# Kernel optimization log

Hardware: AMD Instinct MI355X
Metric: run time of the kernel (lower is better)

The kernel has to match this reference:

```python
import jax, jax.numpy as jnp
import numpy as np

HIDDEN = 1024
HEADS = 16
HEAD_DIM = HIDDEN // HEADS
SCALE = HEAD_DIM ** -0.5


def setup_inputs() -> dict:
    key = jax.random.key(0)
    ks = jax.random.split(key, 7)
    B, N, T = 4, 64, 128
    x = jax.random.normal(ks[0], (B * N, T, HIDDEN), dtype=jnp.float32)
    bvecs = jax.random.normal(ks[1], (B, T, 3), dtype=jnp.float32)
    w_std = HIDDEN ** -0.5
    qkv_w = jax.random.normal(ks[2], (HIDDEN, 3 * HIDDEN), dtype=jnp.float32) * w_std
    qkv_b = jnp.zeros((3 * HIDDEN,), dtype=jnp.float32)
    proj_w = jax.random.normal(ks[3], (HIDDEN, HIDDEN), dtype=jnp.float32) * w_std
    proj_b = jnp.zeros((HIDDEN,), dtype=jnp.float32)
    angular_bias_scale = jnp.ones((1,), dtype=jnp.float32)
    return {"x": x, "bvecs": bvecs, "qkv_w": qkv_w, "qkv_b": qkv_b,
            "proj_w": proj_w, "proj_b": proj_b,
            "angular_bias_scale": angular_bias_scale}


def reference(x, bvecs, qkv_w, qkv_b, proj_w, proj_b, angular_bias_scale):
    BN, T, D = x.shape
    B = bvecs.shape[0]
    N = BN // B
    # QKV projection -> (3, BN, H, T, hd)
    qkv = (x @ qkv_w + qkv_b).reshape(BN, T, 3, HEADS, HEAD_DIM)
    qkv = jnp.transpose(qkv, (2, 0, 3, 1, 4))
    q, k, v = qkv[0], qkv[1], qkv[2]
    # normalize b-vectors and compute per-batch angular cosine similarity (B, T, T)
    bvecs_n = bvecs / (jnp.linalg.norm(bvecs, axis=-1, keepdims=True) + 1e-6)
    cos_sim = jnp.clip(jnp.einsum('bid,bjd->bij', bvecs_n, bvecs_n), -1.0, 1.0)
    # repeat across the N patches per batch -> (BN, 1, T, T)
    angular_bias = jnp.repeat(cos_sim, N, axis=0)[:, None, :, :]
    attn_logits = jnp.einsum('bhid,bhjd->bhij', q, k) * SCALE
    attn = jax.nn.softmax(attn_logits + angular_bias_scale * angular_bias, axis=-1)
    out = jnp.einsum('bhij,bhjd->bhid', attn, v)
    out = jnp.transpose(out, (0, 2, 1, 3)).reshape(BN, T, D)
    return out @ proj_w + proj_b
```

## Files before the change

### kernel.cpp

```cpp
#include <hip/hip_runtime.h>
#include <hip/hip_bf16.h>
#include <stdint.h>


typedef float f32x4 __attribute__((ext_vector_type(4)));
typedef __bf16 bf16x8 __attribute__((ext_vector_type(8)));
typedef unsigned short us8 __attribute__((ext_vector_type(8)));

#define MROWS 32768

static __device__ __forceinline__ unsigned short bfbits(float f) {
  __bf16 h = (__bf16)f;
  return __builtin_bit_cast(unsigned short, h);
}
static __device__ __forceinline__ float bff(unsigned short u) {
  return (float)__builtin_bit_cast(__bf16, u);
}
static __device__ __forceinline__ void gld16(const void* g, void* l) {
  __builtin_amdgcn_global_load_lds(
      (const __attribute__((address_space(1))) void*)g,
      (__attribute__((address_space(3))) void*)l, 16, 0, 0);
}
static __device__ __forceinline__ f32x4 mfma16(bf16x8 a, bf16x8 b, f32x4 c) {
  return __builtin_amdgcn_mfma_f32_16x16x32_bf16(a, b, c, 0, 0, 0);
}

__global__ __launch_bounds__(256) void k_split(const float* __restrict__ x,
                                               unsigned short* __restrict__ xh,
                                               unsigned short* __restrict__ xl,
                                               int n4) {
  int i = blockIdx.x * 256 + threadIdx.x;
  if (i >= n4) return;
  float4 v = ((const float4*)x)[i];
  ushort4 h, l;
  h.x = bfbits(v.x); l.x = bfbits(v.x - bff(h.x));
  h.y = bfbits(v.y); l.y = bfbits(v.y - bff(h.y));
  h.z = bfbits(v.z); l.z = bfbits(v.z - bff(h.z));
  h.w = bfbits(v.w); l.w = bfbits(v.w - bff(h.w));
  ((ushort4*)xh)[i] = h;
  ((ushort4*)xl)[i] = l;
}

__global__ void k_tsplit(const float* __restrict__ w,
                         unsigned short* __restrict__ th,
                         unsigned short* __restrict__ tl_, int K, int N,
                         int remap) {
  __shared__ float tile[32][33];
  int n0 = blockIdx.x * 32, k0 = blockIdx.y * 32;
  int tx = threadIdx.x, ty = threadIdx.y;
#pragma unroll
  for (int j = 0; j < 32; j += 8)
    tile[ty + j][tx] = w[(size_t)(k0 + ty + j) * N + n0 + tx];
  __syncthreads();
#pragma unroll
  for (int j = 0; j < 32; j += 8) {
    float v = tile[tx][ty + j];
    int n = n0 + ty + j;
    int orow = n;
    if (remap) {
      int s = n >> 10, hid = n & 1023;
      orow = (hid >> 8) * 768 + s * 256 + (hid & 255);
    }
    size_t o = (size_t)orow * K + k0 + tx;
    unsigned short hb = bfbits(v);
    th[o] = hb;
    tl_[o] = bfbits(v - bff(hb));
  }
}

__global__ void k_gbias(const float* __restrict__ b, float* __restrict__ gb) {
  int n = blockIdx.x * 256 + threadIdx.x;
  if (n >= 3072) return;
  int s = n >> 10, hid = n & 1023;
  gb[(hid >> 8) * 768 + s * 256 + (hid & 255)] = b[n];
}

__global__ void k_cos(const float* __restrict__ bv, float* __restrict__ cosb) {
  int b = blockIdx.x, t = threadIdx.x;
  __shared__ float nb[128][3];
  float x = bv[(b * 128 + t) * 3 + 0];
  float y = bv[(b * 128 + t) * 3 + 1];
  float z = bv[(b * 128 + t) * 3 + 2];
  float inv = 1.0f / (sqrtf(x * x + y * y + z * z) + 1e-6f);
  nb[t][0] = x * inv; nb[t][1] = y * inv; nb[t][2] = z * inv;
  __syncthreads();
  float xn = nb[t][0], yn = nb[t][1], zn = nb[t][2];
  for (int j = 0; j < 128; j++) {
    float c = xn * nb[j][0] + yn * nb[j][1] + zn * nb[j][2];
    c = fminf(1.0f, fmaxf(-1.0f, c));
    cosb[((size_t)b * 128 + t) * 128 + j] = c;
  }
}

template <int AMODE, int MODE>
__global__ __launch_bounds__(256) void k_gemm(
    const unsigned short* __restrict__ Ah, const unsigned short* __restrict__ Al,
    const float* __restrict__ Af,
    const unsigned short* __restrict__ Bh, const unsigned short* __restrict__ Bl,
    const float* __restrict__ bias, float* __restrict__ C) {
  constexpr int K = 1024;
  __shared__ unsigned short sAh[128 * 32];
  __shared__ unsigned short sAl[128 * 32];
  __shared__ unsigned short sBh[128 * 32];
  __shared__ unsigned short sBl[128 * 32];
  int tid = threadIdx.x;
  int wave = tid >> 6, lane = tid & 63;
  int rowBase = blockIdx.x * 128, colBase = blockIdx.y * 128;
  int wm = wave & 1, wn = wave >> 1;
  int fr = lane & 15, fq = lane >> 4;

  f32x4 acc[4][4];
#pragma unroll
  for (int i = 0; i < 4; i++)
#pragma unroll
    for (int j = 0; j < 4; j++) acc[i][j] = (f32x4){0.f, 0.f, 0.f, 0.f};

  int srow = tid >> 2, scol = (tid & 3) * 8;
  const unsigned short* Bbase = Bh + (size_t)(colBase + srow) * K + scol;
  const unsigned short* Blbase = Bl + (size_t)(colBase + srow) * K + scol;
  const unsigned short* Abase = Ah + (size_t)(rowBase + srow) * K + scol;
  const unsigned short* Albase = Al + (size_t)(rowBase + srow) * K + scol;
  const float* Afbase = Af + (size_t)(rowBase + srow) * K + scol;
  const size_t rstep = (size_t)64 * K;

  for (int kk = 0; kk < K; kk += 32) {
    __syncthreads();
#pragma unroll
    for (int p = 0; p < 2; p++) {
      gld16(Bbase + p * rstep + kk, sBh + p * 2048 + wave * 512);
      gld16(Blbase + p * rstep + kk, sBl + p * 2048 + wave * 512);
    }
    if constexpr (AMODE == 0) {
#pragma unroll
      for (int p = 0; p < 2; p++) {
        gld16(Abase + p * rstep + kk, sAh + p * 2048 + wave * 512);
        gld16(Albase + p * rstep + kk, sAl + p * 2048 + wave * 512);
      }
    } else {
#pragma unroll
      for (int p = 0; p < 2; p++) {
        float4 v0 = *(const float4*)(Afbase + p * rstep + kk);
        float4 v1 = *(const float4*)(Afbase + p * rstep + kk + 4);
        float vv[8] = {v0.x, v0.y, v0.z, v0.w, v1.x, v1.y, v1.z, v1.w};
        us8 hv, lv;
#pragma unroll
        for (int i = 0; i < 8; i++) {
          unsigned short hb = bfbits(vv[i]);
          hv[i] = hb;
          lv[i] = bfbits(vv[i] - bff(hb));
        }
        *(us8*)(sAh + p * 2048 + tid * 8) = hv;
        *(us8*)(sAl + p * 2048 + tid * 8) = lv;
      }
    }
    __syncthreads();

    bf16x8 fah[4], fal[4], fbh[4], fbl[4];
#pragma unroll
    for (int mi = 0; mi < 4; mi++) {
      int r = wm * 64 + mi * 16 + fr;
      fah[mi] = *(const bf16x8*)(sAh + r * 32 + fq * 8);
      fal[mi] = *(const bf16x8*)(sAl + r * 32 + fq * 8);
    }
#pragma unroll
    for (int ni = 0; ni < 4; ni++) {
      int c = wn * 64 + ni * 16 + fr;
      fbh[ni] = *(const bf16x8*)(sBh + c * 32 + fq * 8);
      fbl[ni] = *(const bf16x8*)(sBl + c * 32 + fq * 8);
    }
#pragma unroll
    for (int mi = 0; mi < 4; mi++)
#pragma unroll
      for (int ni = 0; ni < 4; ni++) {
        acc[mi][ni] = mfma16(fah[mi], fbh[ni], acc[mi][ni]);
        acc[mi][ni] = mfma16(fah[mi], fbl[ni], acc[mi][ni]);
        acc[mi][ni] = mfma16(fal[mi], fbh[ni], acc[mi][ni]);
      }
  }

#pragma unroll
  for (int mi = 0; mi < 4; mi++)
#pragma unroll
    for (int ni = 0; ni < 4; ni++)
#pragma unroll
      for (int rr = 0; rr < 4; rr++) {
        int row = rowBase + wm * 64 + mi * 16 + fq * 4 + rr;
        int col = colBase + wn * 64 + ni * 16 + fr;
        float v = acc[mi][ni][rr] + bias[col];
        if constexpr (MODE == 0) {
          int s = col >> 8, hl2 = (col >> 6) & 3, d = col & 63;
          int bn = row >> 7, t = row & 127;
          size_t idx;
          if (s == 2)
            idx = ((size_t)(bn * 4 + hl2) * 64 + d) * 128 + t;
          else
            idx = ((size_t)(bn * 4 + hl2) * 128 + t) * 64 + d;
          C[(size_t)s * 8388608 + idx] = v;
        } else {
          C[(size_t)row * 1024 + col] = v;
        }
      }
}

__global__ __launch_bounds__(256) void k_attn(
    const float* __restrict__ Q, const float* __restrict__ Kb,
    const float* __restrict__ Vt, const float* __restrict__ cosb,
    const float* __restrict__ absSp, unsigned short* __restrict__ Oh,
    unsigned short* __restrict__ Ol, int g) {
  __shared__ __align__(16) unsigned short sQ[2][64 * 72];
  __shared__ __align__(16) unsigned short sKV[2][64 * 72];
  __shared__ __align__(16) float sS[64 * 132];
  unsigned short* sP = (unsigned short*)sS;

  int bx = blockIdx.x;
  int half = bx & 1, hl = (bx >> 1) & 3, bn = bx >> 3, b = bn >> 6;
  int tid = threadIdx.x, wave = tid >> 6, lane = tid & 63;
  int fr = lane & 15, fq = lane >> 4;
  size_t base = (size_t)(bn * 4 + hl) * 8192;
  float absS = absSp[0];

  {
    const float* src = Q + base + (size_t)half * 4096;
#pragma unroll
    for (int p = 0; p < 4; p++) {
      int f = p * 256 + tid, r = f >> 4, c = f & 15;
      float4 v = *(const float4*)(src + r * 64 + c * 4);
      ushort4 h, l;
      h.x = bfbits(v.x); l.x = bfbits(v.x - bff(h.x));
      h.y = bfbits(v.y); l.y = bfbits(v.y - bff(h.y));
      h.z = bfbits(v.z); l.z = bfbits(v.z - bff(h.z));
      h.w = bfbits(v.w); l.w = bfbits(v.w - bff(h.w));
      *(ushort4*)(&sQ[0][r * 72 + c * 4]) = h;
      *(ushort4*)(&sQ[1][r * 72 + c * 4]) = l;
    }
  }

  bf16x8 qh[2], ql[2];

#pragma unroll
  for (int kt = 0; kt < 2; kt++) {
    if (kt) __syncthreads();
    {
      const float* src = Kb + base + (size_t)kt * 4096;
#pragma unroll
      for (int p = 0; p < 4; p++) {
        int f = p * 256 + tid, r = f >> 4, c = f & 15;
        float4 v = *(const float4*)(src + r * 64 + c * 4);
        ushort4 h, l;
        h.x = bfbits(v.x); l.x = bfbits(v.x - bff(h.x));
        h.y = bfbits(v.y); l.y = bfbits(v.y - bff(h.y));
        h.z = bfbits(v.z); l.z = bfbits(v.z - bff(h.z));
        h.w = bfbits(v.w); l.w = bfbits(v.w - bff(h.w));
        *(ushort4*)(&sKV[0][r * 72 + c * 4]) = h;
        *(ushort4*)(&sKV[1][r * 72 + c * 4]) = l;
      }
    }
    __syncthreads();
    if (kt == 0) {
      int rowl = wave * 16 + fr;
#pragma unroll
      for (int ki = 0; ki < 2; ki++) {
        qh[ki] = *(const bf16x8*)(&sQ[0][rowl * 72 + ki * 32 + fq * 8]);
        ql[ki] = *(const bf16x8*)(&sQ[1][rowl * 72 + ki * 32 + fq * 8]);
      }
    }
#pragma unroll
    for (int nt = 0; nt < 4; nt++) {
      f32x4 a = (f32x4){0.f, 0.f, 0.f, 0.f};
      int cl = nt * 16 + fr;
#pragma unroll
      for (int ki = 0; ki < 2; ki++) {
        bf16x8 kh = *(const bf16x8*)(&sKV[0][cl * 72 + ki * 32 + fq * 8]);
        bf16x8 kl = *(const bf16x8*)(&sKV[1][cl * 72 + ki * 32 + fq * 8]);
        a = mfma16(qh[ki], kh, a);
        a = mfma16(qh[ki], kl, a);
        a = mfma16(ql[ki], kh, a);
      }
#pragma unroll
      for (int rr = 0; rr < 4; rr++) {
        int rl = wave * 16 + fq * 4 + rr;
        int col = kt * 64 + nt * 16 + fr;
        int tg = half * 64 + rl;
        float cv = cosb[((size_t)(b * 128 + tg)) * 128 + col];
        sS[rl * 132 + col] = a[rr] * 0.125f + absS * cv;
      }
    }
  }
  __syncthreads();

  {
    const float* src = Vt + base;
#pragma unroll
    for (int p = 0; p < 4; p++) {
      int f = p * 256 + tid, r = f >> 4, c = f & 15;
      float4 v = *(const float4*)(src + r * 128 + c * 4);
      ushort4 h, l;
      h.x = bfbits(v.x); l.x = bfbits(v.x - bff(h.x));
      h.y = bfbits(v.y); l.y = bfbits(v.y - bff(h.y));
      h.z = bfbits(v.z); l.z = bfbits(v.z - bff(h.z));
      h.w = bfbits(v.w); l.w = bfbits(v.w - bff(h.w));
      *(ushort4*)(&sKV[0][r * 72 + c * 4]) = h;
      *(ushort4*)(&sKV[1][r * 72 + c * 4]) = l;
    }
  }

  for (int r = 0; r < 16; r++) {
    int tl = wave * 16 + r;
    float s0 = sS[tl * 132 + lane], s1 = sS[tl * 132 + 64 + lane];
    float m = fmaxf(s0, s1);
#pragma unroll
    for (int off = 32; off >= 1; off >>= 1) m = fmaxf(m, __shfl_xor(m, off));
    float p0 = __expf(s0 - m), p1 = __expf(s1 - m);
    float sum = p0 + p1;
#pragma unroll
    for (int off = 32; off >= 1; off >>= 1) sum += __shfl_xor(sum, off);
    float inv = 1.0f / sum;
    p0 *= inv; p1 *= inv;
    unsigned short h0 = bfbits(p0), h1 = bfbits(p1);
    sP[tl * 264 + lane] = h0;
    sP[tl * 264 + 64 + lane] = h1;
    sP[tl * 264 + 128 + lane] = bfbits(p0 - bff(h0));
    sP[tl * 264 + 192 + lane] = bfbits(p1 - bff(h1));
  }

  f32x4 accO[4];
#pragma unroll
  for (int nt = 0; nt < 4; nt++) accO[nt] = (f32x4){0.f, 0.f, 0.f, 0.f};
#pragma unroll
  for (int vt = 0; vt < 2; vt++) {
    if (vt) {
      __syncthreads();
      const float* src = Vt + base + 64;
#pragma unroll
      for (int p = 0; p < 4; p++) {
        int f = p * 256 + tid, r = f >> 4, c = f & 15;
        float4 v = *(const float4*)(src + r * 128 + c * 4);
        ushort4 h, l;
        h.x = bfbits(v.x); l.x = bfbits(v.x - bff(h.x));
        h.y = bfbits(v.y); l.y = bfbits(v.y - bff(h.y));
        h.z = bfbits(v.z); l.z = bfbits(v.z - bff(h.z));
        h.w = bfbits(v.w); l.w = bfbits(v.w - bff(h.w));
        *(ushort4*)(&sKV[0][r * 72 + c * 4]) = h;
        *(ushort4*)(&sKV[1][r * 72 + c * 4]) = l;
      }
    }
    __syncthreads();
    int rowl = wave * 16 + fr;
    bf16x8 ph[2], pl[2];
#pragma unroll
    for (int ki = 0; ki < 2; ki++) {
      ph[ki] = *(const bf16x8*)(&sP[rowl * 264 + vt * 64 + ki * 32 + fq * 8]);
      pl[ki] = *(const bf16x8*)(&sP[rowl * 264 + 128 + vt * 64 + ki * 32 + fq * 8]);
    }
#pragma unroll
    for (int nt = 0; nt < 4; nt++) {
      int d = nt * 16 + fr;
#pragma unroll
      for (int ki = 0; ki < 2; ki++) {
        bf16x8 vh = *(const bf16x8*)(&sKV[0][d * 72 + ki * 32 + fq * 8]);
        bf16x8 vl = *(const bf16x8*)(&sKV[1][d * 72 + ki * 32 + fq * 8]);
        accO[nt] = mfma16(ph[ki], vh, accO[nt]);
        accO[nt] = mfma16(ph[ki], vl, accO[nt]);
        accO[nt] = mfma16(pl[ki], vh, accO[nt]);
      }
    }
  }

  int hg = g * 4 + hl;
#pragma unroll
  for (int nt = 0; nt < 4; nt++)
#pragma unroll
    for (int rr = 0; rr < 4; rr++) {
      int tl = wave * 16 + fq * 4 + rr;
      int tg = half * 64 + tl;
      int d = nt * 16 + fr;
      float v = accO[nt][rr];
      size_t o = ((size_t)(bn * 128 + tg)) * 1024 + hg * 64 + d;
      unsigned short h = bfbits(v);
      Oh[o] = h;
      Ol[o] = bfbits(v - bff(h));
    }
}

extern "C" void kernel_launch(void* const* d_in, const int* in_sizes, int n_in,
                              void* d_out, int out_size, void* d_ws,
                              size_t ws_size, hipStream_t stream) {
  const float* x = (const float*)d_in[0];
  const float* bv = (const float*)d_in[1];
  const float* qkvw = (const float*)d_in[2];
  const float* qkvb = (const float*)d_in[3];
  const float* projw = (const float*)d_in[4];
  const float* projb = (const float*)d_in[5];
  const float* absS = (const float*)d_in[6];
  float* out = (float*)d_out;

  char* ws = (char*)d_ws;
  size_t off = 0;
  auto alloc = [&](size_t b) {
    char* p = ws + off;
    off += (b + 255) & ~(size_t)255;
    return p;
  };
  unsigned short* wqh = (unsigned short*)alloc((size_t)3072 * 1024 * 2);
  unsigned short* wql = (unsigned short*)alloc((size_t)3072 * 1024 * 2);
  unsigned short* wph = (unsigned short*)alloc((size_t)1024 * 1024 * 2);
  unsigned short* wpl = (unsigned short*)alloc((size_t)1024 * 1024 * 2);
  float* gbias = (float*)alloc(3072 * 4);
  float* cosb = (float*)alloc((size_t)4 * 128 * 128 * 4);
  unsigned short* Oh = (unsigned short*)alloc((size_t)MROWS * 1024 * 2);
  unsigned short* Ol = (unsigned short*)alloc((size_t)MROWS * 1024 * 2);
  unsigned short* xh = (unsigned short*)alloc((size_t)MROWS * 1024 * 2);
  unsigned short* xl = (unsigned short*)alloc((size_t)MROWS * 1024 * 2);
  bool planA = (off <= ws_size);

  float* qg = (float*)d_out;

  k_tsplit<<<dim3(96, 32), dim3(32, 8), 0, stream>>>(qkvw, wqh, wql, 1024, 3072, 1);
  k_tsplit<<<dim3(32, 32), dim3(32, 8), 0, stream>>>(projw, wph, wpl, 1024, 1024, 0);
  k_gbias<<<dim3(12), dim3(256), 0, stream>>>(qkvb, gbias);
  k_cos<<<dim3(4), dim3(128), 0, stream>>>(bv, cosb);
  if (planA)
    k_split<<<dim3(32768), dim3(256), 0, stream>>>(x, xh, xl, 8388608);

  for (int g = 0; g < 4; g++) {
    const unsigned short* bq = wqh + (size_t)g * 768 * 1024;
    const unsigned short* bl = wql + (size_t)g * 768 * 1024;
    if (planA)
      k_gemm<0, 0><<<dim3(256, 6), dim3(256), 0, stream>>>(
          xh, xl, nullptr, bq, bl, gbias + g * 768, qg);
    else
      k_gemm<1, 0><<<dim3(256, 6), dim3(256), 0, stream>>>(
          nullptr, nullptr, x, bq, bl, gbias + g * 768, qg);
    k_attn<<<dim3(2048), dim3(256), 0, stream>>>(
        qg, qg + 8388608, qg + 16777216, cosb, absS, Oh, Ol, g);
  }

  k_gemm<0, 1><<<dim3(256, 8), dim3(256), 0, stream>>>(
      Oh, Ol, nullptr, wph, wpl, projb, out);
}
```

Baseline: 1.441 ms.

## Interleave hi/lo bf16 planes and double-buffer a 128x256 split-bf16 GEMM

The hi and lo bf16 halves of x, the weights and the attention output are now stored interleaved per 32-element K chunk (64 u16 per chunk), so one load brings both planes. The GEMM becomes a 512-thread 128x256 tile with double-buffered LDS, XOR-swizzled shared-memory layout, prefetch of the next K tile issued during MFMA work, setprio hints and an XCD-aware block remap. The goal is to hide global-load latency, avoid LDS bank conflicts and raise MFMA utilisation in the dominant GEMMs. In exchange it uses more LDS (96KB per block), carries more register pressure, and relies on hand-placed barriers and waitcnt that must be correct.

```diff
diff --git a/kernel.cpp b/kernel.cpp
--- a/kernel.cpp
+++ b/kernel.cpp
@@ -6,14 +6,15 @@
 typedef float f32x4 __attribute__((ext_vector_type(4)));
 typedef __bf16 bf16x8 __attribute__((ext_vector_type(8)));
 typedef unsigned short us8 __attribute__((ext_vector_type(8)));
+typedef unsigned short u16;
 
 #define MROWS 32768
 
-static __device__ __forceinline__ unsigned short bfbits(float f) {
+static __device__ __forceinline__ u16 bfbits(float f) {
   __bf16 h = (__bf16)f;
-  return __builtin_bit_cast(unsigned short, h);
-}
-static __device__ __forceinline__ float bff(unsigned short u) {
+  return __builtin_bit_cast(u16, h);
+}
+static __device__ __forceinline__ float bff(u16 u) {
   return (float)__builtin_bit_cast(__bf16, u);
 }
 static __device__ __forceinline__ void gld16(const void* g, void* l) {
@@ -26,9 +27,7 @@
 }
 
 __global__ __launch_bounds__(256) void k_split(const float* __restrict__ x,
-                                               unsigned short* __restrict__ xh,
-                                               unsigned short* __restrict__ xl,
-                                               int n4) {
+                                               u16* __restrict__ xhl, int n4) {
   int i = blockIdx.x * 256 + threadIdx.x;
   if (i >= n4) return;
   float4 v = ((const float4*)x)[i];
@@ -37,14 +36,15 @@
   h.y = bfbits(v.y); l.y = bfbits(v.y - bff(h.y));
   h.z = bfbits(v.z); l.z = bfbits(v.z - bff(h.z));
   h.w = bfbits(v.w); l.w = bfbits(v.w - bff(h.w));
-  ((ushort4*)xh)[i] = h;
-  ((ushort4*)xl)[i] = l;
-}
-
-__global__ void k_tsplit(const float* __restrict__ w,
-                         unsigned short* __restrict__ th,
-                         unsigned short* __restrict__ tl_, int K, int N,
-                         int remap) {
+  int i4 = i << 2;
+  int r = i4 >> 10, k = i4 & 1023;
+  size_t o = ((size_t)r << 11) + (size_t)((k >> 5) << 6) + (k & 31);
+  *(ushort4*)(xhl + o) = h;
+  *(ushort4*)(xhl + o + 32) = l;
+}
+
+__global__ void k_tsplit(const float* __restrict__ w, u16* __restrict__ thl,
+                         int K, int N, int remap) {
   __shared__ float tile[32][33];
   int n0 = blockIdx.x * 32, k0 = blockIdx.y * 32;
   int tx = threadIdx.x, ty = threadIdx.y;
@@ -61,10 +61,11 @@
       int s = n >> 10, hid = n & 1023;
       orow = (hid >> 8) * 768 + s * 256 + (hid & 255);
     }
-    size_t o = (size_t)orow * K + k0 + tx;
-    unsigned short hb = bfbits(v);
-    th[o] = hb;
-    tl_[o] = bfbits(v - bff(hb));
+    int k = k0 + tx;
+    size_t o = ((size_t)orow << 11) + (size_t)((k >> 5) << 6) + (k & 31);
+    u16 hb = bfbits(v);
+    thl[o] = hb;
+    thl[o + 32] = bfbits(v - bff(hb));
   }
 }
 
@@ -93,21 +94,22 @@
 }
 
 template <int AMODE, int MODE>
-__global__ __launch_bounds__(256) void k_gemm(
-    const unsigned short* __restrict__ Ah, const unsigned short* __restrict__ Al,
-    const float* __restrict__ Af,
-    const unsigned short* __restrict__ Bh, const unsigned short* __restrict__ Bl,
-    const float* __restrict__ bias, float* __restrict__ C) {
-  constexpr int K = 1024;
-  __shared__ unsigned short sAh[128 * 32];
-  __shared__ unsigned short sAl[128 * 32];
-  __shared__ unsigned short sBh[128 * 32];
-  __shared__ unsigned short sBl[128 * 32];
+__global__ __launch_bounds__(512, 2) void k_gemm(
+    const u16* __restrict__ Ahl, const float* __restrict__ Af,
+    const u16* __restrict__ Bhl, const float* __restrict__ bias,
+    float* __restrict__ C) {
+  __shared__ __align__(16) u16 sA[2][128 * 64];
+  __shared__ __align__(16) u16 sB[2][256 * 64];
   int tid = threadIdx.x;
   int wave = tid >> 6, lane = tid & 63;
-  int rowBase = blockIdx.x * 128, colBase = blockIdx.y * 128;
-  int wm = wave & 1, wn = wave >> 1;
   int fr = lane & 15, fq = lane >> 4;
+  int wm = wave >> 2, wn = wave & 3;
+
+  int nT = gridDim.y;
+  int h = blockIdx.y * gridDim.x + blockIdx.x;
+  int nwg = gridDim.x * gridDim.y;
+  int w = (h & 7) * (nwg >> 3) + (h >> 3);
+  int rowBase = (w / nT) * 128, colBase = (w % nT) * 256;
 
   f32x4 acc[4][4];
 #pragma unroll
@@ -115,67 +117,97 @@
 #pragma unroll
     for (int j = 0; j < 4; j++) acc[i][j] = (f32x4){0.f, 0.f, 0.f, 0.f};
 
-  int srow = tid >> 2, scol = (tid & 3) * 8;
-  const unsigned short* Bbase = Bh + (size_t)(colBase + srow) * K + scol;
-  const unsigned short* Blbase = Bl + (size_t)(colBase + srow) * K + scol;
-  const unsigned short* Abase = Ah + (size_t)(rowBase + srow) * K + scol;
-  const unsigned short* Albase = Al + (size_t)(rowBase + srow) * K + scol;
-  const float* Afbase = Af + (size_t)(rowBase + srow) * K + scol;
-  const size_t rstep = (size_t)64 * K;
-
-  for (int kk = 0; kk < K; kk += 32) {
-    __syncthreads();
-#pragma unroll
-    for (int p = 0; p < 2; p++) {
-      gld16(Bbase + p * rstep + kk, sBh + p * 2048 + wave * 512);
-      gld16(Blbase + p * rstep + kk, sBl + p * 2048 + wave * 512);
-    }
-    if constexpr (AMODE == 0) {
-#pragma unroll
-      for (int p = 0; p < 2; p++) {
-        gld16(Abase + p * rstep + kk, sAh + p * 2048 + wave * 512);
-        gld16(Albase + p * rstep + kk, sAl + p * 2048 + wave * 512);
-      }
-    } else {
-#pragma unroll
-      for (int p = 0; p < 2; p++) {
-        float4 v0 = *(const float4*)(Afbase + p * rstep + kk);
-        float4 v1 = *(const float4*)(Afbase + p * rstep + kk + 4);
-        float vv[8] = {v0.x, v0.y, v0.z, v0.w, v1.x, v1.y, v1.z, v1.w};
-        us8 hv, lv;
-#pragma unroll
-        for (int i = 0; i < 8; i++) {
-          unsigned short hb = bfbits(vv[i]);
-          hv[i] = hb;
-          lv[i] = bfbits(vv[i] - bff(hb));
+  int lr = lane >> 3, ls = (lane & 7) ^ lr;
+  const u16* aS = Ahl + (size_t)(rowBase + lr) * 2048 + ls * 8;
+  const u16* bS = Bhl + (size_t)(colBase + lr) * 2048 + ls * 8;
+
+  auto stageB = [&](int t, int buf) {
+#pragma unroll
+    for (int q = 0; q < 4; q++) {
+      int R = (q * 8 + wave) * 8;
+      gld16(bS + (size_t)R * 2048 + t * 64, &sB[buf][R * 64]);
+    }
+  };
+  auto stageA0 = [&](int t, int buf) {
+#pragma unroll
+    for (int q = 0; q < 2; q++) {
+      int R = (q * 8 + wave) * 8;
+      gld16(aS + (size_t)R * 2048 + t * 64, &sA[buf][R * 64]);
+    }
+  };
+  auto stageA1 = [&](int t, int buf) {
+    int row = tid >> 2, cs = tid & 3;
+    const float* src = Af + (size_t)(rowBase + row) * 1024 + t * 32 + cs * 8;
+    float4 v0 = *(const float4*)src;
+    float4 v1 = *(const float4*)(src + 4);
+    float vv[8] = {v0.x, v0.y, v0.z, v0.w, v1.x, v1.y, v1.z, v1.w};
+    us8 hv, lv;
+#pragma unroll
+    for (int i = 0; i < 8; i++) {
+      u16 hb = bfbits(vv[i]);
+      hv[i] = hb;
+      lv[i] = bfbits(vv[i] - bff(hb));
+    }
+    int sw = row & 7;
+    *(us8*)(&sA[buf][row * 64 + ((cs ^ sw) << 3)]) = hv;
+    *(us8*)(&sA[buf][row * 64 + (((cs + 4) ^ sw) << 3)]) = lv;
+  };
+
+  auto tile = [&](int t, int cur) {
+    const u16* lA = &sA[cur][0];
+    const u16* lB = &sB[cur][0];
+    bf16x8 fbh[4], fbl[4];
+#pragma unroll
+    for (int p = 0; p < 4; p++) {
+      bf16x8 fah, fal;
+      {
+        int r = wm * 64 + p * 16 + fr;
+        int sw = r & 7;
+        fah = *(const bf16x8*)(&lA[r * 64 + ((fq ^ sw) << 3)]);
+        fal = *(const bf16x8*)(&lA[r * 64 + (((fq + 4) ^ sw) << 3)]);
+      }
+      if (p == 0) {
+#pragma unroll
+        for (int ni = 0; ni < 4; ni++) {
+          int c = wn * 64 + ni * 16 + fr;
+          int sw = c & 7;
+          fbh[ni] = *(const bf16x8*)(&lB[c * 64 + ((fq ^ sw) << 3)]);
+          fbl[ni] = *(const bf16x8*)(&lB[c * 64 + (((fq + 4) ^ sw) << 3)]);
         }
-        *(us8*)(sAh + p * 2048 + tid * 8) = hv;
-        *(us8*)(sAl + p * 2048 + tid * 8) = lv;
-      }
-    }
-    __syncthreads();
-
-    bf16x8 fah[4], fal[4], fbh[4], fbl[4];
-#pragma unroll
-    for (int mi = 0; mi < 4; mi++) {
-      int r = wm * 64 + mi * 16 + fr;
-      fah[mi] = *(const bf16x8*)(sAh + r * 32 + fq * 8);
-      fal[mi] = *(const bf16x8*)(sAl + r * 32 + fq * 8);
-    }
-#pragma unroll
-    for (int ni = 0; ni < 4; ni++) {
-      int c = wn * 64 + ni * 16 + fr;
-      fbh[ni] = *(const bf16x8*)(sBh + c * 32 + fq * 8);
-      fbl[ni] = *(const bf16x8*)(sBl + c * 32 + fq * 8);
-    }
-#pragma unroll
-    for (int mi = 0; mi < 4; mi++)
+        if (t + 1 < 32) {
+          stageB(t + 1, cur ^ 1);
+          if constexpr (AMODE == 0) stageA0(t + 1, cur ^ 1);
+          else stageA1(t + 1, cur ^ 1);
+        }
+      }
+      __builtin_amdgcn_s_barrier();
+      asm volatile("s_waitcnt lgkmcnt(0)" ::: "memory");
+      __builtin_amdgcn_sched_barrier(0);
+      __builtin_amdgcn_s_setprio(1);
 #pragma unroll
       for (int ni = 0; ni < 4; ni++) {
-        acc[mi][ni] = mfma16(fah[mi], fbh[ni], acc[mi][ni]);
-        acc[mi][ni] = mfma16(fah[mi], fbl[ni], acc[mi][ni]);
-        acc[mi][ni] = mfma16(fal[mi], fbh[ni], acc[mi][ni]);
-      }
+        acc[p][ni] = mfma16(fah, fbh[ni], acc[p][ni]);
+        acc[p][ni] = mfma16(fah, fbl[ni], acc[p][ni]);
+        acc[p][ni] = mfma16(fal, fbh[ni], acc[p][ni]);
+      }
+      __builtin_amdgcn_s_setprio(0);
+      if (p == 3) asm volatile("s_waitcnt vmcnt(0)" ::: "memory");
+      __builtin_amdgcn_s_barrier();
+      __builtin_amdgcn_sched_barrier(0);
+    }
+  };
+
+  stageB(0, 0);
+  if constexpr (AMODE == 0) stageA0(0, 0);
+  else stageA1(0, 0);
+  asm volatile("s_waitcnt vmcnt(0) lgkmcnt(0)" ::: "memory");
+  __builtin_amdgcn_s_barrier();
+  __builtin_amdgcn_sched_barrier(0);
+
+#pragma unroll 1
+  for (int tp = 0; tp < 16; tp++) {
+    tile(tp * 2, 0);
+    tile(tp * 2 + 1, 1);
   }
 
 #pragma unroll
@@ -205,12 +237,11 @@
 __global__ __launch_bounds__(256) void k_attn(
     const float* __restrict__ Q, const float* __restrict__ Kb,
     const float* __restrict__ Vt, const float* __restrict__ cosb,
-    const float* __restrict__ absSp, unsigned short* __restrict__ Oh,
-    unsigned short* __restrict__ Ol, int g) {
-  __shared__ __align__(16) unsigned short sQ[2][64 * 72];
-  __shared__ __align__(16) unsigned short sKV[2][64 * 72];
+    const float* __restrict__ absSp, u16* __restrict__ Ohl, int g) {
+  __shared__ __align__(16) u16 sQ[2][64 * 72];
+  __shared__ __align__(16) u16 sKV[2][64 * 72];
   __shared__ __align__(16) float sS[64 * 132];
-  unsigned short* sP = (unsigned short*)sS;
+  u16* sP = (u16*)sS;
 
   int bx = blockIdx.x;
   int half = bx & 1, hl = (bx >> 1) & 3, bn = bx >> 3, b = bn >> 6;
@@ -316,7 +347,7 @@
     for (int off = 32; off >= 1; off >>= 1) sum += __shfl_xor(sum, off);
     float inv = 1.0f / sum;
     p0 *= inv; p1 *= inv;
-    unsigned short h0 = bfbits(p0), h1 = bfbits(p1);
+    u16 h0 = bfbits(p0), h1 = bfbits(p1);
     sP[tl * 264 + lane] = h0;
     sP[tl * 264 + 64 + lane] = h1;
     sP[tl * 264 + 128 + lane] = bfbits(p0 - bff(h0));
@@ -375,10 +406,11 @@
       int tg = half * 64 + tl;
       int d = nt * 16 + fr;
       float v = accO[nt][rr];
-      size_t o = ((size_t)(bn * 128 + tg)) * 1024 + hg * 64 + d;
-      unsigned short h = bfbits(v);
-      Oh[o] = h;
-      Ol[o] = bfbits(v - bff(h));
+      size_t o = ((size_t)(bn * 128 + tg) << 11) +
+                 (size_t)(hg * 2 + (d >> 5)) * 64 + (d & 31);
+      u16 hh = bfbits(v);
+      Ohl[o] = hh;
+      Ohl[o + 32] = bfbits(v - bff(hh));
     }
 }
 
@@ -401,40 +433,35 @@
     off += (b + 255) & ~(size_t)255;
     return p;
   };
-  unsigned short* wqh = (unsigned short*)alloc((size_t)3072 * 1024 * 2);
-  unsigned short* wql = (unsigned short*)alloc((size_t)3072 * 1024 * 2);
-  unsigned short* wph = (unsigned short*)alloc((size_t)1024 * 1024 * 2);
-  unsigned short* wpl = (unsigned short*)alloc((size_t)1024 * 1024 * 2);
+  u16* wqhl = (u16*)alloc((size_t)3072 * 2048 * 2);
+  u16* wphl = (u16*)alloc((size_t)1024 * 2048 * 2);
   float* gbias = (float*)alloc(3072 * 4);
   float* cosb = (float*)alloc((size_t)4 * 128 * 128 * 4);
-  unsigned short* Oh = (unsigned short*)alloc((size_t)MROWS * 1024 * 2);
-  unsigned short* Ol = (unsigned short*)alloc((size_t)MROWS * 1024 * 2);
-  unsigned short* xh = (unsigned short*)alloc((size_t)MROWS * 1024 * 2);
-  unsigned short* xl = (unsigned short*)alloc((size_t)MROWS * 1024 * 2);
+  u16* Ohl = (u16*)alloc((size_t)MROWS * 2048 * 2);
+  u16* xhl = (u16*)alloc((size_t)MROWS * 2048 * 2);
   bool planA = (off <= ws_size);
 
   float* qg = (float*)d_out;
 
-  k_tsplit<<<dim3(96, 32), dim3(32, 8), 0, stream>>>(qkvw, wqh, wql, 1024, 3072, 1);
-  k_tsplit<<<dim3(32, 32), dim3(32, 8), 0, stream>>>(projw, wph, wpl, 1024, 1024, 0);
+  k_tsplit<<<dim3(96, 32), dim3(32, 8), 0, stream>>>(qkvw, wqhl, 1024, 3072, 1);
+  k_tsplit<<<dim3(32, 32), dim3(32, 8), 0, stream>>>(projw, wphl, 1024, 1024, 0);
   k_gbias<<<dim3(12), dim3(256), 0, stream>>>(qkvb, gbias);
   k_cos<<<dim3(4), dim3(128), 0, stream>>>(bv, cosb);
   if (planA)
-    k_split<<<dim3(32768), dim3(256), 0, stream>>>(x, xh, xl, 8388608);
+    k_split<<<dim3(32768), dim3(256), 0, stream>>>(x, xhl, 8388608);
 
   for (int g = 0; g < 4; g++) {
-    const unsigned short* bq = wqh + (size_t)g * 768 * 1024;
-    const unsigned short* bl = wql + (size_t)g * 768 * 1024;
+    const u16* bw = wqhl + (size_t)g * 768 * 2048;
     if (planA)
-      k_gemm<0, 0><<<dim3(256, 6), dim3(256), 0, stream>>>(
-          xh, xl, nullptr, bq, bl, gbias + g * 768, qg);
+      k_gemm<0, 0><<<dim3(256, 3), dim3(512), 0, stream>>>(
+          xhl, nullptr, bw, gbias + g * 768, qg);
     else
-      k_gemm<1, 0><<<dim3(256, 6), dim3(256), 0, stream>>>(
-          nullptr, nullptr, x, bq, bl, gbias + g * 768, qg);
+      k_gemm<1, 0><<<dim3(256, 3), dim3(512), 0, stream>>>(
+          nullptr, x, bw, gbias + g * 768, qg);
     k_attn<<<dim3(2048), dim3(256), 0, stream>>>(
-        qg, qg + 8388608, qg + 16777216, cosb, absS, Oh, Ol, g);
-  }
-
-  k_gemm<0, 1><<<dim3(256, 8), dim3(256), 0, stream>>>(
-      Oh, Ol, nullptr, wph, wpl, projb, out);
-}
+        qg, qg + 8388608, qg + 16777216, cosb, absS, Ohl, g);
+  }
+
+  k_gemm<0, 1><<<dim3(256, 4), dim3(512), 0, stream>>>(
+      Ohl, nullptr, wphl, projb, out);
+}
```

Result: slower. 1.526 ms (+5.9%).
